# Kernel tuning notes

Hardware: AMD Instinct MI355X
Metric: run time of the kernel (lower is better)

Reference implementation:

```python
import jax, jax.numpy as jnp
import numpy as np

S, B, D, E, H, REQ = 2048, 4, 256, 256, 8, 16  # seq, batch, hidden_dim, embed(=hidden_size), heads, band half-width


def setup_inputs() -> dict:
    key = jax.random.key(0)
    ks = jax.random.split(key, 12)
    w = lambda k, shape: jax.random.normal(k, shape, jnp.float32) * 0.02
    return {
        "mod": jax.random.normal(ks[0], (S, B, D), jnp.float32),
        "mask": jnp.zeros((B, S), jnp.float32),  # unused in speaker=False branch (kept for fidelity)
        "Wq": w(ks[1], (E, D)), "bq": jnp.zeros((E,), jnp.float32),
        "Wk": w(ks[2], (E, D)), "bk": jnp.zeros((E,), jnp.float32),
        "Wv": w(ks[3], (E, D)), "bv": jnp.zeros((E,), jnp.float32),
        "Win": w(ks[4], (3 * E, E)), "bin_": jnp.zeros((3 * E,), jnp.float32),  # MHA in_proj
        "Wout": w(ks[5], (E, E)), "bout": jnp.zeros((E,), jnp.float32),         # MHA out_proj
        "Wfc": w(ks[6], (D, E)), "bfc": jnp.zeros((D,), jnp.float32),           # self.fc
        "gamma": jnp.ones((D,), jnp.float32), "beta": jnp.zeros((D,), jnp.float32),
        "req": REQ,
    }


def reference(mod, mask, Wq, bq, Wk, bk, Wv, bv, Win, bin_, Wout, bout, Wfc, bfc, gamma, beta, req):
    s, b, d = mod.shape
    e = Wq.shape[0]
    hd = e // H
    # fc_q/k/v (pre-projection) then MultiheadAttention's own in_proj
    q = mod @ Wq.T + bq                       # (s, b, e)
    k = mod @ Wk.T + bk
    v = mod @ Wv.T + bv
    q = q @ Win[:e].T + bin_[:e]
    k = k @ Win[e:2 * e].T + bin_[e:2 * e]
    v = v @ Win[2 * e:].T + bin_[2 * e:]
    split = lambda x: x.reshape(s, b, H, hd).transpose(1, 2, 0, 3)  # (b, H, s, hd)
    qh, kh, vh = split(q), split(k), split(v)
    scores = jnp.einsum('bhqd,bhkd->bhqk', qh, kh) / jnp.sqrt(jnp.float32(hd))
    idx = jnp.arange(s)
    allowed = jnp.abs(idx[:, None] - idx[None, :]) < req  # band: diag + offsets 1..req-1
    scores = jnp.where(allowed[None, None], scores, -jnp.inf)
    attn = jax.nn.softmax(scores, axis=-1)                # attn dropout = identity (eval)
    ctx = jnp.einsum('bhqk,bhkd->bhqd', attn, vh)
    ctx = ctx.transpose(2, 0, 1, 3).reshape(s, b, e)
    ctx = ctx @ Wout.T + bout
    y = ctx @ Wfc.T + bfc + mod                           # dropout(0.5) = identity (eval), residual
    mu = jnp.mean(y, axis=-1, keepdims=True)
    var = jnp.var(y, axis=-1, keepdims=True)
    return (y - mu) / jnp.sqrt(var + 1e-6) * gamma + beta
```

## Files before the change

### kernel.cpp

```cpp
#include <hip/hip_runtime.h>
#include <hip/hip_bf16.h>
#include <math.h>

#define SS 2048
#define BB 4
#define DD 256
#define EE 256
#define HH 8
#define HD 32
#define TT (SS*BB)

typedef unsigned short ushortt;
typedef __attribute__((ext_vector_type(8))) short short8;
typedef __attribute__((ext_vector_type(4))) float f32x4;

__device__ __forceinline__ float bfbits2f(ushortt u) {
    return __uint_as_float(((unsigned int)u) << 16);
}
__device__ __forceinline__ ushortt f2bf_bits(float f) {
    unsigned int u = __float_as_uint(f);
    unsigned int r = u + 0x7FFFu + ((u >> 16) & 1u);
    return (ushortt)(r >> 16);
}

__device__ __forceinline__ int robust_req(const void* p) {
    int i = *(const int*)p;
    if (i >= 1 && i <= SS) return i;
    float f = __int_as_float(i);
    if (f >= 1.f && f <= (float)SS) return (int)(f + 0.5f);
    float b = bfbits2f(*(const ushortt*)p);
    if (b >= 1.f && b <= (float)SS) return (int)(b + 0.5f);
    return 16;
}

__global__ __launch_bounds__(256)
void fuse_conv(const float* __restrict__ mod,
               const float* __restrict__ Win,
               const float* __restrict__ Wq, const float* __restrict__ Wk,
               const float* __restrict__ Wv,
               const float* __restrict__ bq, const float* __restrict__ bk,
               const float* __restrict__ bv, const float* __restrict__ bin_,
               const float* __restrict__ Wfc, const float* __restrict__ Wout,
               const float* __restrict__ bout, const float* __restrict__ bfc,
               ushortt* __restrict__ Weffb, float* __restrict__ beff,
               ushortt* __restrict__ W2b, float* __restrict__ b2,
               ushortt* __restrict__ modb) {
    __shared__ float red[4];
    const int t = threadIdx.x;

    {
        size_t base = (size_t)blockIdx.x * 2048 + (size_t)t * 8;
        float4 v0 = *(const float4*)(mod + base);
        float4 v1 = *(const float4*)(mod + base + 4);
        ushort4 o0, o1;
        o0.x = f2bf_bits(v0.x); o0.y = f2bf_bits(v0.y);
        o0.z = f2bf_bits(v0.z); o0.w = f2bf_bits(v0.w);
        o1.x = f2bf_bits(v1.x); o1.y = f2bf_bits(v1.y);
        o1.z = f2bf_bits(v1.z); o1.w = f2bf_bits(v1.w);
        *(ushort4*)(modb + base)     = o0;
        *(ushort4*)(modb + base + 4) = o1;
    }

    float tb;
    if (blockIdx.x < 3 * EE) {
        int r = blockIdx.x;
        int i = r / EE;
        const float* Wi = (i == 0) ? Wq : ((i == 1) ? Wk : Wv);
        const float* bi = (i == 0) ? bq : ((i == 1) ? bk : bv);
        float acc = 0.f;
        for (int e1 = 0; e1 < EE; ++e1) acc += Win[r * EE + e1] * Wi[e1 * DD + t];
        Weffb[(size_t)r * DD + t] = f2bf_bits(acc);
        tb = Win[r * EE + t] * bi[t];
    } else {
        int d = blockIdx.x - 3 * EE;
        float acc = 0.f;
        for (int e = 0; e < EE; ++e) acc += Wfc[d * EE + e] * Wout[e * EE + t];
        W2b[(size_t)d * EE + t] = f2bf_bits(acc);
        tb = Wfc[d * EE + t] * bout[t];
    }
#pragma unroll
    for (int off = 32; off >= 1; off >>= 1) tb += __shfl_xor(tb, off);
    if ((t & 63) == 0) red[t >> 6] = tb;
    __syncthreads();
    if (t == 0) {
        float s = red[0] + red[1] + red[2] + red[3];
        if (blockIdx.x < 3 * EE) beff[blockIdx.x] = s + bin_[blockIdx.x];
        else                     b2[blockIdx.x - 3 * EE] = s + bfc[blockIdx.x - 3 * EE];
    }
}

__global__ __launch_bounds__(256)
void gemm_qkv(const ushortt* __restrict__ A, const ushortt* __restrict__ Bw,
              const float* __restrict__ bias, ushortt* __restrict__ C) {
    __shared__ __align__(16) ushortt Alds[64][72];
    __shared__ __align__(16) ushortt Blds[192][72];
    const int t    = threadIdx.x;
    const int lane = t & 63;
    const int w    = t >> 6;
    const int quad = lane >> 4;
    const int l16  = lane & 15;
    const int n0   = blockIdx.x * 192;
    const int m0   = blockIdx.y * 64;
    const int N    = 3 * EE, K = DD;

    f32x4 acc[4][3];
#pragma unroll
    for (int fm = 0; fm < 4; ++fm)
#pragma unroll
        for (int fn = 0; fn < 3; ++fn) acc[fm][fn] = (f32x4){0.f,0.f,0.f,0.f};

    for (int k0 = 0; k0 < K; k0 += 64) {
        {
            int row = t >> 2, c8 = (t & 3) * 8;
            const ushortt* ap = A + (size_t)(m0 + row) * K + k0;
            *(float4*)&Alds[row][c8]      = *(const float4*)(ap + c8);
            *(float4*)&Alds[row][c8 + 32] = *(const float4*)(ap + c8 + 32);
        }
#pragma unroll
        for (int i = 0; i < 6; ++i) {
            int slot = t + 256 * i;
            int row = slot >> 3, c8 = (slot & 7) * 8;
            *(float4*)&Blds[row][c8] = *(const float4*)(Bw + (size_t)(n0 + row) * K + k0 + c8);
        }
        __syncthreads();
        short8 af[4][2], bfr[3][2];
#pragma unroll
        for (int fm = 0; fm < 4; ++fm)
#pragma unroll
            for (int kf = 0; kf < 2; ++kf)
                af[fm][kf] = *(const short8*)&Alds[fm * 16 + l16][kf * 32 + quad * 8];
#pragma unroll
        for (int fn = 0; fn < 3; ++fn)
#pragma unroll
            for (int kf = 0; kf < 2; ++kf)
                bfr[fn][kf] = *(const short8*)&Blds[w * 48 + fn * 16 + l16][kf * 32 + quad * 8];
#pragma unroll
        for (int kf = 0; kf < 2; ++kf)
#pragma unroll
            for (int fm = 0; fm < 4; ++fm)
#pragma unroll
                for (int fn = 0; fn < 3; ++fn)
                    acc[fm][fn] = __builtin_amdgcn_mfma_f32_16x16x32_bf16(
                        af[fm][kf], bfr[fn][kf], acc[fm][fn], 0, 0, 0);
        __syncthreads();
    }
#pragma unroll
    for (int fm = 0; fm < 4; ++fm)
#pragma unroll
        for (int fn = 0; fn < 3; ++fn)
#pragma unroll
            for (int r = 0; r < 4; ++r) {
                int row = m0 + fm * 16 + quad * 4 + r;
                int col = n0 + w * 48 + fn * 16 + l16;
                C[(size_t)row * N + col] = f2bf_bits(acc[fm][fn][r] + bias[col]);
            }
}

__global__ __launch_bounds__(256)
void attn_mfma(const ushortt* __restrict__ qkv,
               const void* __restrict__ reqp,
               ushortt* __restrict__ ctx) {
    __shared__ __align__(16) ushortt Plds[4][16 * 72];
    const int t    = threadIdx.x;
    const int w    = t >> 6;
    const int lane = t & 63;
    const int l16  = lane & 15;
    const int quad = lane >> 4;
    const int wid  = blockIdx.x * 4 + w;
    const int stile = wid >> 5;
    const int rem   = wid & 31;
    const int b = rem >> 3;
    const int h = rem & 7;
    const int s0 = stile * 16;
    const int req = robust_req(reqp);

    const ushortt* qptr = qkv + ((size_t)(s0 + l16) * BB + b) * (3 * EE) + h * HD + quad * 8;
    short8 aq = *(const short8*)qptr;

    f32x4 sc[3];
#pragma unroll
    for (int kt = 0; kt < 3; ++kt) {
        int j = s0 - 16 + kt * 16 + l16;
        int jc = min(max(j, 0), SS - 1);
        const ushortt* kp = qkv + ((size_t)jc * BB + b) * (3 * EE) + EE + h * HD + quad * 8;
        short8 bk = *(const short8*)kp;
        sc[kt] = __builtin_amdgcn_mfma_f32_16x16x32_bf16(aq, bk, (f32x4){0.f,0.f,0.f,0.f}, 0, 0, 0);
    }

    const float scale = 0.17677669529663687f;
    float pv[3][4];
#pragma unroll
    for (int r = 0; r < 4; ++r) {
        int s = s0 + quad * 4 + r;
        float vv[3];
        float mx = -INFINITY;
#pragma unroll
        for (int kt = 0; kt < 3; ++kt) {
            int j = s0 - 16 + kt * 16 + l16;
            int dj = s - j;
            bool valid = (j >= 0) && (j < SS) && (dj < req) && (-dj < req);
            vv[kt] = valid ? sc[kt][r] * scale : -INFINITY;
            mx = fmaxf(mx, vv[kt]);
        }
#pragma unroll
        for (int off = 1; off <= 8; off <<= 1) mx = fmaxf(mx, __shfl_xor(mx, off));
        float sum = 0.f;
#pragma unroll
        for (int kt = 0; kt < 3; ++kt) {
            float p = (vv[kt] > -INFINITY) ? __expf(vv[kt] - mx) : 0.f;
            pv[kt][r] = p;
            sum += p;
        }
#pragma unroll
        for (int off = 1; off <= 8; off <<= 1) sum += __shfl_xor(sum, off);
        float inv = 1.f / sum;
#pragma unroll
        for (int kt = 0; kt < 3; ++kt) pv[kt][r] *= inv;
    }

    ushortt* P = &Plds[w][0];
#pragma unroll
    for (int kt = 0; kt < 3; ++kt)
#pragma unroll
        for (int r = 0; r < 4; ++r)
            P[(quad * 4 + r) * 72 + kt * 16 + l16] = f2bf_bits(pv[kt][r]);
#pragma unroll
    for (int r = 0; r < 4; ++r)
        P[(quad * 4 + r) * 72 + 48 + l16] = 0;
    __syncthreads();

    short8 pa[2];
    pa[0] = *(const short8*)&P[l16 * 72 + quad * 8];
    pa[1] = *(const short8*)&P[l16 * 72 + 32 + quad * 8];

    f32x4 acc[2];
    acc[0] = (f32x4){0.f,0.f,0.f,0.f};
    acc[1] = (f32x4){0.f,0.f,0.f,0.f};
#pragma unroll
    for (int c = 0; c < 2; ++c) {
#pragma unroll
        for (int nd = 0; nd < 2; ++nd) {
            short8 bv;
#pragma unroll
            for (int u = 0; u < 8; ++u) {
                int j = s0 - 16 + c * 32 + quad * 8 + u;
                int jc = min(max(j, 0), SS - 1);
                bv[u] = (short)qkv[((size_t)jc * BB + b) * (3 * EE) + 2 * EE + h * HD + nd * 16 + l16];
            }
            acc[nd] = __builtin_amdgcn_mfma_f32_16x16x32_bf16(pa[c], bv, acc[nd], 0, 0, 0);
        }
    }

#pragma unroll
    for (int nd = 0; nd < 2; ++nd)
#pragma unroll
        for (int r = 0; r < 4; ++r) {
            int tok = (s0 + quad * 4 + r) * BB + b;
            ctx[(size_t)tok * EE + h * HD + nd * 16 + l16] = f2bf_bits(acc[nd][r]);
        }
}

__global__ __launch_bounds__(256)
void gemm_tail_ln(const ushortt* __restrict__ A, const ushortt* __restrict__ Bw,
                  const float* __restrict__ b2, const float* __restrict__ mod,
                  const float* __restrict__ gamma, const float* __restrict__ beta,
                  float* __restrict__ out) {
    __shared__ __align__(16) ushortt Alds[32][72];
    __shared__ __align__(16) ushortt Blds[256][72];
    __shared__ float part1[4][32], part2[4][32];
    const int t    = threadIdx.x;
    const int lane = t & 63;
    const int w    = t >> 6;
    const int quad = lane >> 4;
    const int l16  = lane & 15;
    const int m0   = blockIdx.x * 32;
    const int K    = EE;

    f32x4 acc[2][4];
#pragma unroll
    for (int fm = 0; fm < 2; ++fm)
#pragma unroll
        for (int fn = 0; fn < 4; ++fn) acc[fm][fn] = (f32x4){0.f,0.f,0.f,0.f};

    for (int k0 = 0; k0 < K; k0 += 64) {
        {
            int row = t >> 3, c8 = (t & 7) * 8;
            *(float4*)&Alds[row][c8] = *(const float4*)(A + (size_t)(m0 + row) * K + k0 + c8);
        }
#pragma unroll
        for (int i = 0; i < 8; ++i) {
            int slot = t + 256 * i;
            int row = slot >> 3, c8 = (slot & 7) * 8;
            *(float4*)&Blds[row][c8] = *(const float4*)(Bw + (size_t)row * K + k0 + c8);
        }
        __syncthreads();
        short8 af[2][2], bfr[4][2];
#pragma unroll
        for (int fm = 0; fm < 2; ++fm)
#pragma unroll
            for (int kf = 0; kf < 2; ++kf)
                af[fm][kf] = *(const short8*)&Alds[fm * 16 + l16][kf * 32 + quad * 8];
#pragma unroll
        for (int fn = 0; fn < 4; ++fn)
#pragma unroll
            for (int kf = 0; kf < 2; ++kf)
                bfr[fn][kf] = *(const short8*)&Blds[w * 64 + fn * 16 + l16][kf * 32 + quad * 8];
#pragma unroll
        for (int kf = 0; kf < 2; ++kf)
#pragma unroll
            for (int fm = 0; fm < 2; ++fm)
#pragma unroll
                for (int fn = 0; fn < 4; ++fn)
                    acc[fm][fn] = __builtin_amdgcn_mfma_f32_16x16x32_bf16(
                        af[fm][kf], bfr[fn][kf], acc[fm][fn], 0, 0, 0);
        __syncthreads();
    }

#pragma unroll
    for (int fm = 0; fm < 2; ++fm) {
#pragma unroll
        for (int r = 0; r < 4; ++r) {
            int rowl = fm * 16 + quad * 4 + r;
            int row  = m0 + rowl;
            float s1 = 0.f, s2 = 0.f;
#pragma unroll
            for (int fn = 0; fn < 4; ++fn) {
                int col = w * 64 + fn * 16 + l16;
                float v = acc[fm][fn][r] + b2[col] + mod[(size_t)row * DD + col];
                acc[fm][fn][r] = v;
                s1 += v;
                s2 += v * v;
            }
#pragma unroll
            for (int off = 1; off <= 8; off <<= 1) {
                s1 += __shfl_xor(s1, off);
                s2 += __shfl_xor(s2, off);
            }
            if (l16 == 0) { part1[w][rowl] = s1; part2[w][rowl] = s2; }
        }
    }
    __syncthreads();
#pragma unroll
    for (int fm = 0; fm < 2; ++fm) {
#pragma unroll
        for (int r = 0; r < 4; ++r) {
            int rowl = fm * 16 + quad * 4 + r;
            int row  = m0 + rowl;
            float S1 = part1[0][rowl] + part1[1][rowl] + part1[2][rowl] + part1[3][rowl];
            float S2 = part2[0][rowl] + part2[1][rowl] + part2[2][rowl] + part2[3][rowl];
            float mean = S1 * (1.f / DD);
            float var  = S2 * (1.f / DD) - mean * mean;
            float inv  = rsqrtf(var + 1e-6f);
#pragma unroll
            for (int fn = 0; fn < 4; ++fn) {
                int col = w * 64 + fn * 16 + l16;
                out[(size_t)row * DD + col] = (acc[fm][fn][r] - mean) * inv * gamma[col] + beta[col];
            }
        }
    }
}

extern "C" void kernel_launch(void* const* d_in, const int* in_sizes, int n_in,
                              void* d_out, int out_size, void* d_ws, size_t ws_size,
                              hipStream_t stream) {
    const float* mod  = (const float*)d_in[0];
    const float* Wq   = (const float*)d_in[2];
    const float* bq   = (const float*)d_in[3];
    const float* Wk   = (const float*)d_in[4];
    const float* bk   = (const float*)d_in[5];
    const float* Wv   = (const float*)d_in[6];
    const float* bv   = (const float*)d_in[7];
    const float* Win  = (const float*)d_in[8];
    const float* bin_ = (const float*)d_in[9];
    const float* Wout = (const float*)d_in[10];
    const float* bout = (const float*)d_in[11];
    const float* Wfc  = (const float*)d_in[12];
    const float* bfc  = (const float*)d_in[13];
    const float* gamma= (const float*)d_in[14];
    const float* beta = (const float*)d_in[15];
    const void*  reqp = d_in[16];

    float* out = (float*)d_out;

    float*  beff = (float*)d_ws;
    float*  b2   = beff + 3 * EE;
    ushortt* Weffb = (ushortt*)(b2 + DD);
    ushortt* W2b   = Weffb + 3 * EE * DD;
    ushortt* modb  = W2b + DD * EE;
    ushortt* qkvb  = modb + (size_t)TT * DD;
    ushortt* ctxb  = qkvb + (size_t)TT * 3 * EE;

    fuse_conv<<<1024, 256, 0, stream>>>(mod, Win, Wq, Wk, Wv, bq, bk, bv, bin_,
                                        Wfc, Wout, bout, bfc,
                                        Weffb, beff, W2b, b2, modb);
    gemm_qkv<<<dim3(4, TT / 64), 256, 0, stream>>>(modb, Weffb, beff, qkvb);
    attn_mfma<<<4096 / 4, 256, 0, stream>>>(qkvb, reqp, ctxb);
    gemm_tail_ln<<<TT / 32, 256, 0, stream>>>(ctxb, W2b, b2, mod, gamma, beta, out);
}
```

Measured before the change: 129.4 us.

## Fuse attention with output GEMM and LayerNorm; retile QKV GEMM to 64x96

The attention kernel and the tail GEMM plus LayerNorm become one kernel. Each block handles 16 tokens of one batch across all 8 heads, keeps the context tile in LDS, and multiplies it by W2 read directly from global memory, so the ctx buffer no longer goes through HBM and one launch is removed. The QKV GEMM tile shrinks from 64x192 to 64x96 with a 2x2 wave layout, doubling the grid for better occupancy. In exchange, each fused block repeatedly reads W2 from global/L2 without LDS staging. Heads are processed in two serial rounds per wave, which lowers attention parallelism.

```diff
diff --git a/kernel.cpp b/kernel.cpp
--- a/kernel.cpp
+++ b/kernel.cpp
@@ -93,19 +93,20 @@
 void gemm_qkv(const ushortt* __restrict__ A, const ushortt* __restrict__ Bw,
               const float* __restrict__ bias, ushortt* __restrict__ C) {
     __shared__ __align__(16) ushortt Alds[64][72];
-    __shared__ __align__(16) ushortt Blds[192][72];
+    __shared__ __align__(16) ushortt Blds[96][72];
     const int t    = threadIdx.x;
     const int lane = t & 63;
     const int w    = t >> 6;
+    const int wm   = w >> 1, wn = w & 1;
     const int quad = lane >> 4;
     const int l16  = lane & 15;
-    const int n0   = blockIdx.x * 192;
+    const int n0   = blockIdx.x * 96;
     const int m0   = blockIdx.y * 64;
     const int N    = 3 * EE, K = DD;
 
-    f32x4 acc[4][3];
-#pragma unroll
-    for (int fm = 0; fm < 4; ++fm)
+    f32x4 acc[2][3];
+#pragma unroll
+    for (int fm = 0; fm < 2; ++fm)
 #pragma unroll
         for (int fn = 0; fn < 3; ++fn) acc[fm][fn] = (f32x4){0.f,0.f,0.f,0.f};
 
@@ -117,27 +118,27 @@
             *(float4*)&Alds[row][c8 + 32] = *(const float4*)(ap + c8 + 32);
         }
 #pragma unroll
-        for (int i = 0; i < 6; ++i) {
+        for (int i = 0; i < 3; ++i) {
             int slot = t + 256 * i;
             int row = slot >> 3, c8 = (slot & 7) * 8;
             *(float4*)&Blds[row][c8] = *(const float4*)(Bw + (size_t)(n0 + row) * K + k0 + c8);
         }
         __syncthreads();
-        short8 af[4][2], bfr[3][2];
-#pragma unroll
-        for (int fm = 0; fm < 4; ++fm)
+        short8 af[2][2], bfr[3][2];
+#pragma unroll
+        for (int fm = 0; fm < 2; ++fm)
 #pragma unroll
             for (int kf = 0; kf < 2; ++kf)
-                af[fm][kf] = *(const short8*)&Alds[fm * 16 + l16][kf * 32 + quad * 8];
+                af[fm][kf] = *(const short8*)&Alds[wm * 32 + fm * 16 + l16][kf * 32 + quad * 8];
 #pragma unroll
         for (int fn = 0; fn < 3; ++fn)
 #pragma unroll
             for (int kf = 0; kf < 2; ++kf)
-                bfr[fn][kf] = *(const short8*)&Blds[w * 48 + fn * 16 + l16][kf * 32 + quad * 8];
+                bfr[fn][kf] = *(const short8*)&Blds[wn * 48 + fn * 16 + l16][kf * 32 + quad * 8];
 #pragma unroll
         for (int kf = 0; kf < 2; ++kf)
 #pragma unroll
-            for (int fm = 0; fm < 4; ++fm)
+            for (int fm = 0; fm < 2; ++fm)
 #pragma unroll
                 for (int fn = 0; fn < 3; ++fn)
                     acc[fm][fn] = __builtin_amdgcn_mfma_f32_16x16x32_bf16(
@@ -145,217 +146,178 @@
         __syncthreads();
     }
 #pragma unroll
-    for (int fm = 0; fm < 4; ++fm)
+    for (int fm = 0; fm < 2; ++fm)
 #pragma unroll
         for (int fn = 0; fn < 3; ++fn)
 #pragma unroll
             for (int r = 0; r < 4; ++r) {
-                int row = m0 + fm * 16 + quad * 4 + r;
-                int col = n0 + w * 48 + fn * 16 + l16;
+                int row = m0 + wm * 32 + fm * 16 + quad * 4 + r;
+                int col = n0 + wn * 48 + fn * 16 + l16;
                 C[(size_t)row * N + col] = f2bf_bits(acc[fm][fn][r] + bias[col]);
             }
 }
 
 __global__ __launch_bounds__(256)
-void attn_mfma(const ushortt* __restrict__ qkv,
+void attn_tail(const ushortt* __restrict__ qkv,
                const void* __restrict__ reqp,
-               ushortt* __restrict__ ctx) {
+               const ushortt* __restrict__ W2b, const float* __restrict__ b2,
+               const float* __restrict__ mod,
+               const float* __restrict__ gamma, const float* __restrict__ beta,
+               float* __restrict__ out) {
+    __shared__ __align__(16) ushortt ctx[16][264];
     __shared__ __align__(16) ushortt Plds[4][16 * 72];
+    __shared__ float part1[4][16], part2[4][16];
     const int t    = threadIdx.x;
     const int w    = t >> 6;
     const int lane = t & 63;
     const int l16  = lane & 15;
     const int quad = lane >> 4;
-    const int wid  = blockIdx.x * 4 + w;
-    const int stile = wid >> 5;
-    const int rem   = wid & 31;
-    const int b = rem >> 3;
-    const int h = rem & 7;
-    const int s0 = stile * 16;
-    const int req = robust_req(reqp);
-
-    const ushortt* qptr = qkv + ((size_t)(s0 + l16) * BB + b) * (3 * EE) + h * HD + quad * 8;
-    short8 aq = *(const short8*)qptr;
-
-    f32x4 sc[3];
-#pragma unroll
-    for (int kt = 0; kt < 3; ++kt) {
-        int j = s0 - 16 + kt * 16 + l16;
-        int jc = min(max(j, 0), SS - 1);
-        const ushortt* kp = qkv + ((size_t)jc * BB + b) * (3 * EE) + EE + h * HD + quad * 8;
-        short8 bk = *(const short8*)kp;
-        sc[kt] = __builtin_amdgcn_mfma_f32_16x16x32_bf16(aq, bk, (f32x4){0.f,0.f,0.f,0.f}, 0, 0, 0);
-    }
-
+    const int stile = blockIdx.x >> 2;
+    const int b     = blockIdx.x & 3;
+    const int s0    = stile * 16;
+    const int req   = robust_req(reqp);
     const float scale = 0.17677669529663687f;
-    float pv[3][4];
-#pragma unroll
-    for (int r = 0; r < 4; ++r) {
-        int s = s0 + quad * 4 + r;
-        float vv[3];
-        float mx = -INFINITY;
+
+#pragma unroll 1
+    for (int rnd = 0; rnd < 2; ++rnd) {
+        int h = rnd * 4 + w;
+
+        const ushortt* qptr = qkv + ((size_t)(s0 + l16) * BB + b) * (3 * EE) + h * HD + quad * 8;
+        short8 aq = *(const short8*)qptr;
+
+        f32x4 sc[3];
 #pragma unroll
         for (int kt = 0; kt < 3; ++kt) {
             int j = s0 - 16 + kt * 16 + l16;
-            int dj = s - j;
-            bool valid = (j >= 0) && (j < SS) && (dj < req) && (-dj < req);
-            vv[kt] = valid ? sc[kt][r] * scale : -INFINITY;
-            mx = fmaxf(mx, vv[kt]);
-        }
-#pragma unroll
-        for (int off = 1; off <= 8; off <<= 1) mx = fmaxf(mx, __shfl_xor(mx, off));
-        float sum = 0.f;
-#pragma unroll
-        for (int kt = 0; kt < 3; ++kt) {
-            float p = (vv[kt] > -INFINITY) ? __expf(vv[kt] - mx) : 0.f;
-            pv[kt][r] = p;
-            sum += p;
-        }
-#pragma unroll
-        for (int off = 1; off <= 8; off <<= 1) sum += __shfl_xor(sum, off);
-        float inv = 1.f / sum;
-#pragma unroll
-        for (int kt = 0; kt < 3; ++kt) pv[kt][r] *= inv;
-    }
-
-    ushortt* P = &Plds[w][0];
-#pragma unroll
-    for (int kt = 0; kt < 3; ++kt)
+            int jc = min(max(j, 0), SS - 1);
+            const ushortt* kp = qkv + ((size_t)jc * BB + b) * (3 * EE) + EE + h * HD + quad * 8;
+            short8 bk = *(const short8*)kp;
+            sc[kt] = __builtin_amdgcn_mfma_f32_16x16x32_bf16(aq, bk, (f32x4){0.f,0.f,0.f,0.f}, 0, 0, 0);
+        }
+
+        float pv[3][4];
+#pragma unroll
+        for (int r = 0; r < 4; ++r) {
+            int s = s0 + quad * 4 + r;
+            float vv[3];
+            float mx = -INFINITY;
+#pragma unroll
+            for (int kt = 0; kt < 3; ++kt) {
+                int j = s0 - 16 + kt * 16 + l16;
+                int dj = s - j;
+                bool valid = (j >= 0) && (j < SS) && (dj < req) && (-dj < req);
+                vv[kt] = valid ? sc[kt][r] * scale : -INFINITY;
+                mx = fmaxf(mx, vv[kt]);
+            }
+#pragma unroll
+            for (int off = 1; off <= 8; off <<= 1) mx = fmaxf(mx, __shfl_xor(mx, off));
+            float sum = 0.f;
+#pragma unroll
+            for (int kt = 0; kt < 3; ++kt) {
+                float p = (vv[kt] > -INFINITY) ? __expf(vv[kt] - mx) : 0.f;
+                pv[kt][r] = p;
+                sum += p;
+            }
+#pragma unroll
+            for (int off = 1; off <= 8; off <<= 1) sum += __shfl_xor(sum, off);
+            float inv = 1.f / sum;
+#pragma unroll
+            for (int kt = 0; kt < 3; ++kt) pv[kt][r] *= inv;
+        }
+
+        ushortt* P = &Plds[w][0];
+#pragma unroll
+        for (int kt = 0; kt < 3; ++kt)
+#pragma unroll
+            for (int r = 0; r < 4; ++r)
+                P[(quad * 4 + r) * 72 + kt * 16 + l16] = f2bf_bits(pv[kt][r]);
 #pragma unroll
         for (int r = 0; r < 4; ++r)
-            P[(quad * 4 + r) * 72 + kt * 16 + l16] = f2bf_bits(pv[kt][r]);
-#pragma unroll
-    for (int r = 0; r < 4; ++r)
-        P[(quad * 4 + r) * 72 + 48 + l16] = 0;
+            P[(quad * 4 + r) * 72 + 48 + l16] = 0;
+
+        short8 pa[2];
+        pa[0] = *(const short8*)&P[l16 * 72 + quad * 8];
+        pa[1] = *(const short8*)&P[l16 * 72 + 32 + quad * 8];
+
+        f32x4 acc2[2];
+        acc2[0] = (f32x4){0.f,0.f,0.f,0.f};
+        acc2[1] = (f32x4){0.f,0.f,0.f,0.f};
+#pragma unroll
+        for (int c = 0; c < 2; ++c) {
+#pragma unroll
+            for (int nd = 0; nd < 2; ++nd) {
+                short8 bv;
+#pragma unroll
+                for (int u = 0; u < 8; ++u) {
+                    int j = s0 - 16 + c * 32 + quad * 8 + u;
+                    int jc = min(max(j, 0), SS - 1);
+                    bv[u] = (short)qkv[((size_t)jc * BB + b) * (3 * EE) + 2 * EE + h * HD + nd * 16 + l16];
+                }
+                acc2[nd] = __builtin_amdgcn_mfma_f32_16x16x32_bf16(pa[c], bv, acc2[nd], 0, 0, 0);
+            }
+        }
+#pragma unroll
+        for (int nd = 0; nd < 2; ++nd)
+#pragma unroll
+            for (int r = 0; r < 4; ++r)
+                ctx[quad * 4 + r][h * 32 + nd * 16 + l16] = f2bf_bits(acc2[nd][r]);
+    }
     __syncthreads();
 
-    short8 pa[2];
-    pa[0] = *(const short8*)&P[l16 * 72 + quad * 8];
-    pa[1] = *(const short8*)&P[l16 * 72 + 32 + quad * 8];
-
-    f32x4 acc[2];
-    acc[0] = (f32x4){0.f,0.f,0.f,0.f};
-    acc[1] = (f32x4){0.f,0.f,0.f,0.f};
-#pragma unroll
-    for (int c = 0; c < 2; ++c) {
-#pragma unroll
-        for (int nd = 0; nd < 2; ++nd) {
-            short8 bv;
-#pragma unroll
-            for (int u = 0; u < 8; ++u) {
-                int j = s0 - 16 + c * 32 + quad * 8 + u;
-                int jc = min(max(j, 0), SS - 1);
-                bv[u] = (short)qkv[((size_t)jc * BB + b) * (3 * EE) + 2 * EE + h * HD + nd * 16 + l16];
-            }
-            acc[nd] = __builtin_amdgcn_mfma_f32_16x16x32_bf16(pa[c], bv, acc[nd], 0, 0, 0);
-        }
-    }
-
-#pragma unroll
-    for (int nd = 0; nd < 2; ++nd)
-#pragma unroll
-        for (int r = 0; r < 4; ++r) {
-            int tok = (s0 + quad * 4 + r) * BB + b;
-            ctx[(size_t)tok * EE + h * HD + nd * 16 + l16] = f2bf_bits(acc[nd][r]);
-        }
-}
-
-__global__ __launch_bounds__(256)
-void gemm_tail_ln(const ushortt* __restrict__ A, const ushortt* __restrict__ Bw,
-                  const float* __restrict__ b2, const float* __restrict__ mod,
-                  const float* __restrict__ gamma, const float* __restrict__ beta,
-                  float* __restrict__ out) {
-    __shared__ __align__(16) ushortt Alds[32][72];
-    __shared__ __align__(16) ushortt Blds[256][72];
-    __shared__ float part1[4][32], part2[4][32];
-    const int t    = threadIdx.x;
-    const int lane = t & 63;
-    const int w    = t >> 6;
-    const int quad = lane >> 4;
-    const int l16  = lane & 15;
-    const int m0   = blockIdx.x * 32;
-    const int K    = EE;
-
-    f32x4 acc[2][4];
-#pragma unroll
-    for (int fm = 0; fm < 2; ++fm)
-#pragma unroll
-        for (int fn = 0; fn < 4; ++fn) acc[fm][fn] = (f32x4){0.f,0.f,0.f,0.f};
-
-    for (int k0 = 0; k0 < K; k0 += 64) {
-        {
-            int row = t >> 3, c8 = (t & 7) * 8;
-            *(float4*)&Alds[row][c8] = *(const float4*)(A + (size_t)(m0 + row) * K + k0 + c8);
-        }
-#pragma unroll
-        for (int i = 0; i < 8; ++i) {
-            int slot = t + 256 * i;
-            int row = slot >> 3, c8 = (slot & 7) * 8;
-            *(float4*)&Blds[row][c8] = *(const float4*)(Bw + (size_t)row * K + k0 + c8);
-        }
-        __syncthreads();
-        short8 af[2][2], bfr[4][2];
-#pragma unroll
-        for (int fm = 0; fm < 2; ++fm)
-#pragma unroll
-            for (int kf = 0; kf < 2; ++kf)
-                af[fm][kf] = *(const short8*)&Alds[fm * 16 + l16][kf * 32 + quad * 8];
-#pragma unroll
-        for (int fn = 0; fn < 4; ++fn)
-#pragma unroll
-            for (int kf = 0; kf < 2; ++kf)
-                bfr[fn][kf] = *(const short8*)&Blds[w * 64 + fn * 16 + l16][kf * 32 + quad * 8];
+    f32x4 tacc[4];
+#pragma unroll
+    for (int fn = 0; fn < 4; ++fn) tacc[fn] = (f32x4){0.f,0.f,0.f,0.f};
+
+#pragma unroll
+    for (int k0 = 0; k0 < EE; k0 += 64) {
+        short8 af[2];
 #pragma unroll
         for (int kf = 0; kf < 2; ++kf)
-#pragma unroll
-            for (int fm = 0; fm < 2; ++fm)
-#pragma unroll
-                for (int fn = 0; fn < 4; ++fn)
-                    acc[fm][fn] = __builtin_amdgcn_mfma_f32_16x16x32_bf16(
-                        af[fm][kf], bfr[fn][kf], acc[fm][fn], 0, 0, 0);
-        __syncthreads();
-    }
-
-#pragma unroll
-    for (int fm = 0; fm < 2; ++fm) {
-#pragma unroll
-        for (int r = 0; r < 4; ++r) {
-            int rowl = fm * 16 + quad * 4 + r;
-            int row  = m0 + rowl;
-            float s1 = 0.f, s2 = 0.f;
+            af[kf] = *(const short8*)&ctx[l16][k0 + kf * 32 + quad * 8];
+#pragma unroll
+        for (int kf = 0; kf < 2; ++kf)
 #pragma unroll
             for (int fn = 0; fn < 4; ++fn) {
-                int col = w * 64 + fn * 16 + l16;
-                float v = acc[fm][fn][r] + b2[col] + mod[(size_t)row * DD + col];
-                acc[fm][fn][r] = v;
-                s1 += v;
-                s2 += v * v;
-            }
-#pragma unroll
-            for (int off = 1; off <= 8; off <<= 1) {
-                s1 += __shfl_xor(s1, off);
-                s2 += __shfl_xor(s2, off);
-            }
-            if (l16 == 0) { part1[w][rowl] = s1; part2[w][rowl] = s2; }
-        }
+                int colrow = w * 64 + fn * 16 + l16;
+                short8 bfr = *(const short8*)(W2b + (size_t)colrow * EE + k0 + kf * 32 + quad * 8);
+                tacc[fn] = __builtin_amdgcn_mfma_f32_16x16x32_bf16(af[kf], bfr, tacc[fn], 0, 0, 0);
+            }
+    }
+
+#pragma unroll
+    for (int r = 0; r < 4; ++r) {
+        int rowl = quad * 4 + r;
+        size_t tok = (size_t)(s0 + rowl) * BB + b;
+        float s1 = 0.f, s2 = 0.f;
+#pragma unroll
+        for (int fn = 0; fn < 4; ++fn) {
+            int col = w * 64 + fn * 16 + l16;
+            float v = tacc[fn][r] + b2[col] + mod[tok * DD + col];
+            tacc[fn][r] = v;
+            s1 += v;
+            s2 += v * v;
+        }
+#pragma unroll
+        for (int off = 1; off <= 8; off <<= 1) {
+            s1 += __shfl_xor(s1, off);
+            s2 += __shfl_xor(s2, off);
+        }
+        if (l16 == 0) { part1[w][rowl] = s1; part2[w][rowl] = s2; }
     }
     __syncthreads();
 #pragma unroll
-    for (int fm = 0; fm < 2; ++fm) {
-#pragma unroll
-        for (int r = 0; r < 4; ++r) {
-            int rowl = fm * 16 + quad * 4 + r;
-            int row  = m0 + rowl;
-            float S1 = part1[0][rowl] + part1[1][rowl] + part1[2][rowl] + part1[3][rowl];
-            float S2 = part2[0][rowl] + part2[1][rowl] + part2[2][rowl] + part2[3][rowl];
-            float mean = S1 * (1.f / DD);
-            float var  = S2 * (1.f / DD) - mean * mean;
-            float inv  = rsqrtf(var + 1e-6f);
-#pragma unroll
-            for (int fn = 0; fn < 4; ++fn) {
-                int col = w * 64 + fn * 16 + l16;
-                out[(size_t)row * DD + col] = (acc[fm][fn][r] - mean) * inv * gamma[col] + beta[col];
-            }
+    for (int r = 0; r < 4; ++r) {
+        int rowl = quad * 4 + r;
+        size_t tok = (size_t)(s0 + rowl) * BB + b;
+        float S1 = part1[0][rowl] + part1[1][rowl] + part1[2][rowl] + part1[3][rowl];
+        float S2 = part2[0][rowl] + part2[1][rowl] + part2[2][rowl] + part2[3][rowl];
+        float mean = S1 * (1.f / DD);
+        float var  = S2 * (1.f / DD) - mean * mean;
+        float inv  = rsqrtf(var + 1e-6f);
+#pragma unroll
+        for (int fn = 0; fn < 4; ++fn) {
+            int col = w * 64 + fn * 16 + l16;
+            out[tok * DD + col] = (tacc[fn][r] - mean) * inv * gamma[col] + beta[col];
         }
     }
 }
@@ -388,12 +350,11 @@
     ushortt* W2b   = Weffb + 3 * EE * DD;
     ushortt* modb  = W2b + DD * EE;
     ushortt* qkvb  = modb + (size_t)TT * DD;
-    ushortt* ctxb  = qkvb + (size_t)TT * 3 * EE;
 
     fuse_conv<<<1024, 256, 0, stream>>>(mod, Win, Wq, Wk, Wv, bq, bk, bv, bin_,
                                         Wfc, Wout, bout, bfc,
                                         Weffb, beff, W2b, b2, modb);
-    gemm_qkv<<<dim3(4, TT / 64), 256, 0, stream>>>(modb, Weffb, beff, qkvb);
-    attn_mfma<<<4096 / 4, 256, 0, stream>>>(qkvb, reqp, ctxb);
-    gemm_tail_ln<<<TT / 32, 256, 0, stream>>>(ctxb, W2b, b2, mod, gamma, beta, out);
-}
+    gemm_qkv<<<dim3(8, TT / 64), 256, 0, stream>>>(modb, Weffb, beff, qkvb);
+    attn_tail<<<SS / 16 * BB, 256, 0, stream>>>(qkvb, reqp, W2b, b2, mod,
+                                                gamma, beta, out);
+}
```

Result: slower. 137.4 us (+6.2%).

## Restructure QKV GEMM: A fragments in registers, full-K B tile in LDS

Applied to the files above, without the earlier changes.

The QKV projection GEMM now loads each wave's 16-row slice of A straight from global memory into registers for the full K=256, and stages a 96-column by full-K slice of B in LDS once, with no K loop. This removes the per-K-step barriers and the A staging through LDS. The N tile is halved from 192 to 96, doubling the grid to 8x128 blocks, which adds parallelism but means each A row is read from global memory by twice as many blocks. The B LDS tile grows to about 50KB, which may limit how many blocks fit per CU.

```diff
diff --git a/kernel.cpp b/kernel.cpp
--- a/kernel.cpp
+++ b/kernel.cpp
@@ -92,68 +92,51 @@
 __global__ __launch_bounds__(256)
 void gemm_qkv(const ushortt* __restrict__ A, const ushortt* __restrict__ Bw,
               const float* __restrict__ bias, ushortt* __restrict__ C) {
-    __shared__ __align__(16) ushortt Alds[64][72];
-    __shared__ __align__(16) ushortt Blds[192][72];
+    __shared__ __align__(16) ushortt Blds[96][264];
     const int t    = threadIdx.x;
     const int lane = t & 63;
     const int w    = t >> 6;
     const int quad = lane >> 4;
     const int l16  = lane & 15;
-    const int n0   = blockIdx.x * 192;
+    const int n0   = blockIdx.x * 96;
     const int m0   = blockIdx.y * 64;
     const int N    = 3 * EE, K = DD;
 
-    f32x4 acc[4][3];
-#pragma unroll
-    for (int fm = 0; fm < 4; ++fm)
-#pragma unroll
-        for (int fn = 0; fn < 3; ++fn) acc[fm][fn] = (f32x4){0.f,0.f,0.f,0.f};
-
-    for (int k0 = 0; k0 < K; k0 += 64) {
-        {
-            int row = t >> 2, c8 = (t & 3) * 8;
-            const ushortt* ap = A + (size_t)(m0 + row) * K + k0;
-            *(float4*)&Alds[row][c8]      = *(const float4*)(ap + c8);
-            *(float4*)&Alds[row][c8 + 32] = *(const float4*)(ap + c8 + 32);
-        }
-#pragma unroll
-        for (int i = 0; i < 6; ++i) {
-            int slot = t + 256 * i;
-            int row = slot >> 3, c8 = (slot & 7) * 8;
-            *(float4*)&Blds[row][c8] = *(const float4*)(Bw + (size_t)(n0 + row) * K + k0 + c8);
-        }
-        __syncthreads();
-        short8 af[4][2], bfr[3][2];
-#pragma unroll
-        for (int fm = 0; fm < 4; ++fm)
-#pragma unroll
-            for (int kf = 0; kf < 2; ++kf)
-                af[fm][kf] = *(const short8*)&Alds[fm * 16 + l16][kf * 32 + quad * 8];
-#pragma unroll
-        for (int fn = 0; fn < 3; ++fn)
-#pragma unroll
-            for (int kf = 0; kf < 2; ++kf)
-                bfr[fn][kf] = *(const short8*)&Blds[w * 48 + fn * 16 + l16][kf * 32 + quad * 8];
-#pragma unroll
-        for (int kf = 0; kf < 2; ++kf)
-#pragma unroll
-            for (int fm = 0; fm < 4; ++fm)
-#pragma unroll
-                for (int fn = 0; fn < 3; ++fn)
-                    acc[fm][fn] = __builtin_amdgcn_mfma_f32_16x16x32_bf16(
-                        af[fm][kf], bfr[fn][kf], acc[fm][fn], 0, 0, 0);
-        __syncthreads();
-    }
-#pragma unroll
-    for (int fm = 0; fm < 4; ++fm)
-#pragma unroll
-        for (int fn = 0; fn < 3; ++fn)
-#pragma unroll
-            for (int r = 0; r < 4; ++r) {
-                int row = m0 + fm * 16 + quad * 4 + r;
-                int col = n0 + w * 48 + fn * 16 + l16;
-                C[(size_t)row * N + col] = f2bf_bits(acc[fm][fn][r] + bias[col]);
-            }
+    short8 af[8];
+    const ushortt* arow = A + (size_t)(m0 + w * 16 + l16) * K + quad * 8;
+#pragma unroll
+    for (int kf = 0; kf < 8; ++kf)
+        af[kf] = *(const short8*)(arow + kf * 32);
+
+#pragma unroll
+    for (int i = 0; i < 12; ++i) {
+        int slot = t + 256 * i;
+        int row  = slot >> 5;
+        int c8   = (slot & 31) * 8;
+        *(float4*)&Blds[row][c8] = *(const float4*)(Bw + (size_t)(n0 + row) * K + c8);
+    }
+    __syncthreads();
+
+    f32x4 acc[6];
+#pragma unroll
+    for (int fn = 0; fn < 6; ++fn) acc[fn] = (f32x4){0.f, 0.f, 0.f, 0.f};
+
+#pragma unroll
+    for (int fn = 0; fn < 6; ++fn)
+#pragma unroll
+        for (int kf = 0; kf < 8; ++kf) {
+            short8 bfr = *(const short8*)&Blds[fn * 16 + l16][kf * 32 + quad * 8];
+            acc[fn] = __builtin_amdgcn_mfma_f32_16x16x32_bf16(af[kf], bfr, acc[fn], 0, 0, 0);
+        }
+
+#pragma unroll
+    for (int fn = 0; fn < 6; ++fn)
+#pragma unroll
+        for (int r = 0; r < 4; ++r) {
+            int row = m0 + w * 16 + quad * 4 + r;
+            int col = n0 + fn * 16 + l16;
+            C[(size_t)row * N + col] = f2bf_bits(acc[fn][r] + bias[col]);
+        }
 }
 
 __global__ __launch_bounds__(256)
@@ -393,7 +376,7 @@
     fuse_conv<<<1024, 256, 0, stream>>>(mod, Win, Wq, Wk, Wv, bq, bk, bv, bin_,
                                         Wfc, Wout, bout, bfc,
                                         Weffb, beff, W2b, b2, modb);
-    gemm_qkv<<<dim3(4, TT / 64), 256, 0, stream>>>(modb, Weffb, beff, qkvb);
+    gemm_qkv<<<dim3(8, TT / 64), 256, 0, stream>>>(modb, Weffb, beff, qkvb);
     attn_mfma<<<4096 / 4, 256, 0, stream>>>(qkvb, reqp, ctxb);
     gemm_tail_ln<<<TT / 32, 256, 0, stream>>>(ctxb, W2b, b2, mod, gamma, beta, out);
 }
```

Measured after the change: 134.1 us. 3.7% more time.
